# Kernel tuning notes

Measured on AMD Instinct MI355X. Metric: run time of the kernel, lower is better.

## Reference

```python
import jax, jax.numpy as jnp
import numpy as np

B, T, D, H, V = 256, 32, 500, 1024, 8000
NF = 512  # conv output channels per window size


def setup_inputs() -> dict:
    key = jax.random.key(0)
    ks = jax.random.split(key, 20)
    s = 0.02
    inp = {
        "text": jax.random.normal(ks[0], (B, T, D), jnp.float32),
        "text_bow": jax.random.uniform(ks[1], (B, V), jnp.float32),
        "text_lengths": jax.random.randint(ks[2], (B,), 1, T + 1).astype(jnp.int32),
        # GRU forward direction (PyTorch layout: [3H, D], [3H, H], gates r,z,n)
        "Wih_f": jax.random.normal(ks[3], (3 * H, D), jnp.float32) * s,
        "Whh_f": jax.random.normal(ks[4], (3 * H, H), jnp.float32) * s,
        "bih_f": jax.random.normal(ks[5], (3 * H,), jnp.float32) * s,
        "bhh_f": jax.random.normal(ks[6], (3 * H,), jnp.float32) * s,
        # GRU backward direction
        "Wih_b": jax.random.normal(ks[7], (3 * H, D), jnp.float32) * s,
        "Whh_b": jax.random.normal(ks[8], (3 * H, H), jnp.float32) * s,
        "bih_b": jax.random.normal(ks[9], (3 * H,), jnp.float32) * s,
        "bhh_b": jax.random.normal(ks[10], (3 * H,), jnp.float32) * s,
        # reduce linear: 2H -> H
        "W_red": jax.random.normal(ks[11], (H, 2 * H), jnp.float32) * s,
        "b_red": jax.random.normal(ks[12], (H,), jnp.float32) * s,
        # conv kernels, reshaped from Conv2d [512,1,ws,2H] to 1D conv [512, 2H, ws]
        "conv_w2": jax.random.normal(ks[13], (NF, 2 * H, 2), jnp.float32) * s,
        "conv_b2": jax.random.normal(ks[14], (NF,), jnp.float32) * s,
        "conv_w3": jax.random.normal(ks[15], (NF, 2 * H, 3), jnp.float32) * s,
        "conv_b3": jax.random.normal(ks[16], (NF,), jnp.float32) * s,
        "conv_w4": jax.random.normal(ks[17], (NF, 2 * H, 4), jnp.float32) * s,
        "conv_b4": jax.random.normal(ks[18], (NF,), jnp.float32) * s,
    }
    return inp


def _run_gru_dir(x, lengths, Wih, Whh, bih, bhh, reverse):
    """One GRU direction over padded [B,T,D] with packed-sequence semantics:
    outputs are zero at t >= length (as pad_packed_sequence produces)."""
    b, t, _ = x.shape
    h_dim = Whh.shape[1]
    xg = jnp.einsum('btd,gd->btg', x, Wih) + bih  # [B,T,3H] input projections
    valid = jnp.arange(t)[None, :] < lengths[:, None]  # [B,T]

    def step(h, inp):
        xg_t, v = inp  # [B,3H], [B]
        hg = h @ Whh.T + bhh
        xr, xz, xn = jnp.split(xg_t, 3, axis=-1)
        hr, hz, hn = jnp.split(hg, 3, axis=-1)
        r = jax.nn.sigmoid(xr + hr)
        z = jax.nn.sigmoid(xz + hz)
        n = jnp.tanh(xn + r * hn)
        h_new = (1.0 - z) * n + z * h
        h_new = jnp.where(v[:, None], h_new, h)
        out = jnp.where(v[:, None], h_new, 0.0)
        return h_new, out

    h0 = jnp.zeros((b, h_dim), x.dtype)
    xs = (jnp.swapaxes(xg, 0, 1), valid.T)  # time-major
    _, outs = jax.lax.scan(step, h0, xs, reverse=reverse)
    return jnp.swapaxes(outs, 0, 1)  # [B,T,H]


def _conv_branch(x_c, w, b, ws):
    # x_c: [B, 2H, T]; w: [512, 2H, ws]; 'same-padding-both-sides' (ws-1) like Conv2d padding=(ws-1,0)
    y = jax.lax.conv_general_dilated(
        x_c, w, window_strides=(1,), padding=[(ws - 1, ws - 1)],
        dimension_numbers=('NCH', 'OIH', 'NCH')) + b[None, :, None]
    y = jax.nn.leaky_relu(y, 0.01)
    return jnp.max(y, axis=-1)  # global max-pool over time -> [B,512]


def reference(text, text_bow, text_lengths, Wih_f, Whh_f, bih_f, bhh_f,
              Wih_b, Whh_b, bih_b, bhh_b, W_red, b_red,
              conv_w2, conv_b2, conv_w3, conv_b3, conv_w4, conv_b4):
    out_f = _run_gru_dir(text, text_lengths, Wih_f, Whh_f, bih_f, bhh_f, reverse=False)
    out_b = _run_gru_dir(text, text_lengths, Wih_b, Whh_b, bih_b, bhh_b, reverse=True)
    gru_init_out = jnp.concatenate([out_f, out_b], axis=-1)  # [B,T,2H]

    # masked mean pooling over valid timesteps (the per-sample Python loop)
    mask = (jnp.arange(gru_init_out.shape[1])[None, :] < text_lengths[:, None]).astype(gru_init_out.dtype)
    gru_mean = jnp.sum(gru_init_out * mask[:, :, None], axis=1) / text_lengths[:, None].astype(gru_init_out.dtype)
    gru_out = gru_mean @ W_red.T + b_red  # [B,H] (dropout is identity at eval)

    x_c = jnp.swapaxes(gru_init_out, 1, 2)  # [B,2H,T]
    con_out = jnp.concatenate([
        _conv_branch(x_c, conv_w2, conv_b2, 2),
        _conv_branch(x_c, conv_w3, conv_b3, 3),
        _conv_branch(x_c, conv_w4, conv_b4, 4),
    ], axis=1)  # [B,1536]

    return jnp.concatenate([gru_out, con_out, text_bow], axis=1)  # [B, H+1536+V]
```

## Files before the change

### kernel.cpp

```cpp
#include <hip/hip_runtime.h>
#include <hip/hip_bf16.h>
#include <math.h>

#define B_ 256
#define T_ 32
#define D_ 500
#define H_ 1024
#define V_ 8000
#define NF_ 512
#define G3H (3*H_)
#define G6H (6*H_)
#define H2 (2*H_)
#define OUTC (H_ + 3*NF_ + V_)
#define KPAD 512
#define NTAP 9
#define NCAT (NTAP*NF_)
#define MS 512
#define WFRAG_G (64*32*512)
#define WHH_N (3*64*32*64)

typedef float f32x4 __attribute__((ext_vector_type(4)));
typedef short bf16x8 __attribute__((ext_vector_type(8)));

static __device__ __forceinline__ short f2b(float f) {
    unsigned u = __float_as_uint(f);
    unsigned r = (u + 0x7fffu + ((u >> 16) & 1u)) >> 16;
    return (short)r;
}
static __device__ __forceinline__ float b2f(short s) {
    return __uint_as_float(((unsigned)(unsigned short)s) << 16);
}

__global__ __launch_bounds__(256) void gemm_bt(
    const short* __restrict__ A, int lda,
    const short* __restrict__ Bt, int ldb,
    const float* __restrict__ bias,
    void* __restrict__ Cv, int ldc,
    int K, int mode)
{
    __shared__ short As[128 * 32];
    __shared__ short Bs[128 * 32];
    const int tid  = threadIdx.x;
    const int w    = tid >> 6, lane = tid & 63;

    const int nbx = gridDim.x;
    const int nwg = nbx * gridDim.y;
    int flat = blockIdx.y * nbx + blockIdx.x;
    flat = (flat & 7) * (nwg >> 3) + (flat >> 3);
    const int m0 = (flat / nbx) * 128, n0 = (flat % nbx) * 128;

    const int wm   = (w >> 1) * 64, wn = (w & 1) * 64;

    f32x4 acc[4][4];
#pragma unroll
    for (int i = 0; i < 4; ++i)
#pragma unroll
        for (int j = 0; j < 4; ++j) acc[i][j] = (f32x4){0.f, 0.f, 0.f, 0.f};

    const int srow = w * 16 + (lane >> 2);
    const int scol = (lane & 3) * 8;
    const long aoff0 = (long)(m0 + srow) * lda + scol;
    const long aoff1 = (long)(m0 + srow + 64) * lda + scol;
    const long boff0 = (long)(n0 + srow) * ldb + scol;
    const long boff1 = (long)(n0 + srow + 64) * ldb + scol;
    short* lA0 = As + w * 512;        short* lA1 = As + 2048 + w * 512;
    short* lB0 = Bs + w * 512;        short* lB1 = Bs + 2048 + w * 512;

    const int fr = lane & 15, fk = (lane >> 4) * 8;

    for (int kt = 0; kt < K; kt += 32) {
        __builtin_amdgcn_global_load_lds((const __attribute__((address_space(1))) void*)(A + aoff0 + kt),
                                         (__attribute__((address_space(3))) void*)lA0, 16, 0, 0);
        __builtin_amdgcn_global_load_lds((const __attribute__((address_space(1))) void*)(A + aoff1 + kt),
                                         (__attribute__((address_space(3))) void*)lA1, 16, 0, 0);
        __builtin_amdgcn_global_load_lds((const __attribute__((address_space(1))) void*)(Bt + boff0 + kt),
                                         (__attribute__((address_space(3))) void*)lB0, 16, 0, 0);
        __builtin_amdgcn_global_load_lds((const __attribute__((address_space(1))) void*)(Bt + boff1 + kt),
                                         (__attribute__((address_space(3))) void*)lB1, 16, 0, 0);
        __syncthreads();
        bf16x8 af[4], bfv[4];
#pragma unroll
        for (int i = 0; i < 4; ++i) af[i]  = *(const bf16x8*)(As + (wm + i * 16 + fr) * 32 + fk);
#pragma unroll
        for (int j = 0; j < 4; ++j) bfv[j] = *(const bf16x8*)(Bs + (wn + j * 16 + fr) * 32 + fk);
#pragma unroll
        for (int i = 0; i < 4; ++i)
#pragma unroll
            for (int j = 0; j < 4; ++j)
                acc[i][j] = __builtin_amdgcn_mfma_f32_16x16x32_bf16(af[i], bfv[j], acc[i][j], 0, 0, 0);
        __syncthreads();
    }

    const int er = (lane >> 4) * 4;
    const int ec = lane & 15;
#pragma unroll
    for (int i = 0; i < 4; ++i) {
#pragma unroll
        for (int j = 0; j < 4; ++j) {
#pragma unroll
            for (int q = 0; q < 4; ++q) {
                const int m = m0 + wm + i * 16 + er + q;
                const int n = n0 + wn + j * 16 + ec;
                float v = acc[i][j][q];
                if (mode == 0) {
                    ((float*)Cv)[(long)m * ldc + n] = v + bias[n];
                } else if (mode == 2) {
                    ((short*)Cv)[(long)m * ldc + n] = f2b(v + bias[n]);
                } else {
                    ((_Float16*)Cv)[(long)m * ldc + n] = (_Float16)v;
                }
            }
        }
    }
}

__global__ void repack_whh2(const float* __restrict__ srcf,
                            const float* __restrict__ srcb,
                            short* __restrict__ dst)
{
    const int idx = blockIdx.x * 256 + threadIdx.x;
    const int h = idx >= WHH_N;
    const int local = idx - h * WHH_N;
    const float* src = h ? srcb : srcf;
    const int l = local & 63;
    const int kt = (local >> 6) & 31;
    const int j16 = (local >> 11) & 63;
    const int g = local >> 17;
    const long srow = ((long)(g << 10) + (j16 << 4) + (l & 15)) * H_ + kt * 32 + ((l >> 4) << 3);
    short o[8];
#pragma unroll
    for (int e = 0; e < 8; ++e) o[e] = f2b(src[srow + e]);
    *(bf16x8*)&dst[(long)idx * 8] = *(bf16x8*)o;
}

__global__ __launch_bounds__(512) void gru_step_frag(
    const short* __restrict__ hbf_prev, short* __restrict__ hbf_next,
    const float* __restrict__ h32_prev, float* __restrict__ h32_next,
    const short* __restrict__ wfragf, const short* __restrict__ wfragb,
    const float* __restrict__ bhhf, const float* __restrict__ bhhb,
    const short* __restrict__ xgcat,
    short* __restrict__ gout, const int* __restrict__ lengths, int s)
{
    __shared__ f32x4 lacc[4][6][64];
    const int tid = threadIdx.x;
    const int w8 = tid >> 6;
    const int w = w8 & 3;
    const int khalf = w8 >> 2;
    const int lane = tid & 63;
    const int bid = blockIdx.x;
    const int jt = bid & 31;
    const int mtd = bid >> 5;
    const int dir = mtd >> 2, mt = mtd & 3;
    const int m0 = dir * 256 + mt * 64;
    const int j0 = jt * 32;
    const int wm = (w >> 1) * 32, wj = (w & 1) * 16;
    const int tt = dir ? (T_ - 1 - s) : s;

    const short* wfrag = dir ? wfragb : wfragf;
    const float* bhh = dir ? bhhb : bhhf;

    const int fr15 = lane & 15, fk8 = (lane >> 4) * 8;
    const long arow0 = (long)(m0 + wm + fr15) * H_ + fk8 + khalf * 512;
    const long arow1 = arow0 + (long)16 * H_;
    const int j16 = (j0 + wj) >> 4;
    const short* bbase = wfrag + ((long)j16 * 32 + khalf * 16) * 512 + lane * 8;

    f32x4 acc[3][2];
#pragma unroll
    for (int g = 0; g < 3; ++g)
#pragma unroll
        for (int i = 0; i < 2; ++i) acc[g][i] = (f32x4){0.f, 0.f, 0.f, 0.f};

#pragma unroll 4
    for (int kt = 0; kt < 16; ++kt) {
        const bf16x8 af0 = *(const bf16x8*)(hbf_prev + arow0 + kt * 32);
        const bf16x8 af1 = *(const bf16x8*)(hbf_prev + arow1 + kt * 32);
        const bf16x8 b0 = *(const bf16x8*)(bbase + (long)kt * 512);
        const bf16x8 b1 = *(const bf16x8*)(bbase + (long)kt * 512 + WFRAG_G);
        const bf16x8 b2 = *(const bf16x8*)(bbase + (long)kt * 512 + 2 * WFRAG_G);
        acc[0][0] = __builtin_amdgcn_mfma_f32_16x16x32_bf16(af0, b0, acc[0][0], 0, 0, 0);
        acc[0][1] = __builtin_amdgcn_mfma_f32_16x16x32_bf16(af1, b0, acc[0][1], 0, 0, 0);
        acc[1][0] = __builtin_amdgcn_mfma_f32_16x16x32_bf16(af0, b1, acc[1][0], 0, 0, 0);
        acc[1][1] = __builtin_amdgcn_mfma_f32_16x16x32_bf16(af1, b1, acc[1][1], 0, 0, 0);
        acc[2][0] = __builtin_amdgcn_mfma_f32_16x16x32_bf16(af0, b2, acc[2][0], 0, 0, 0);
        acc[2][1] = __builtin_amdgcn_mfma_f32_16x16x32_bf16(af1, b2, acc[2][1], 0, 0, 0);
    }

    if (khalf == 1) {
#pragma unroll
        for (int g = 0; g < 3; ++g)
#pragma unroll
            for (int i = 0; i < 2; ++i)
                lacc[w][g * 2 + i][lane] = acc[g][i];
    }
    __syncthreads();
    if (khalf == 1) return;

#pragma unroll
    for (int g = 0; g < 3; ++g)
#pragma unroll
        for (int i = 0; i < 2; ++i)
            acc[g][i] += lacc[w][g * 2 + i][lane];

    const int er = (lane >> 4) * 4, ec = lane & 15;
    const int jj = j0 + wj + ec;
    const float bhr = bhh[jj], bhz = bhh[H_ + jj], bhn = bhh[2 * H_ + jj];

#pragma unroll
    for (int i = 0; i < 2; ++i) {
#pragma unroll
        for (int q = 0; q < 4; ++q) {
            const int m = m0 + wm + i * 16 + er + q;
            const int b = m & 255;
            const short* xrow = xgcat + ((long)b * T_ + tt) * G6H + (long)dir * G3H;
            const float xr = b2f(xrow[jj]);
            const float xz = b2f(xrow[H_ + jj]);
            const float xn = b2f(xrow[2 * H_ + jj]);
            const float rr = 1.f / (1.f + expf(-(xr + acc[0][i][q] + bhr)));
            const float zz = 1.f / (1.f + expf(-(xz + acc[1][i][q] + bhz)));
            const float nn = tanhf(xn + rr * (acc[2][i][q] + bhn));
            const long hidx = (long)m * H_ + jj;
            const float hp = h32_prev[hidx];
            const float hnew = (1.f - zz) * nn + zz * hp;
            const bool valid = tt < lengths[b];
            const float ho = valid ? hnew : hp;
            h32_next[hidx] = ho;
            hbf_next[hidx] = f2b(ho);
            gout[((long)b * T_ + tt) * H2 + (long)dir * H_ + jj] = valid ? f2b(hnew) : (short)0;
        }
    }
}

__global__ void f2b_pad(const float* __restrict__ src, short* __restrict__ dst,
                        int Ksrc, int Kdst)
{
    const int idx = blockIdx.x * 256 + threadIdx.x;
    const int r = idx / Kdst, c = idx % Kdst;
    dst[idx] = (c < Ksrc) ? f2b(src[(long)r * Ksrc + c]) : (short)0;
}

__global__ void wih_pad2(const float* __restrict__ a, const float* __restrict__ b,
                         short* __restrict__ dst)
{
    const int idx = blockIdx.x * 256 + threadIdx.x;
    const int h = idx >= G3H * KPAD;
    const int rem = idx - h * G3H * KPAD;
    const int r = rem / KPAD, c = rem % KPAD;
    const float* s = h ? b : a;
    dst[idx] = (c < D_) ? f2b(s[(long)r * D_ + c]) : (short)0;
}

__global__ void cat_bias(const float* __restrict__ a, const float* __restrict__ b,
                         float* __restrict__ dst)
{
    const int idx = blockIdx.x * 256 + threadIdx.x;
    dst[idx] = (idx < G3H) ? a[idx] : b[idx - G3H];
}

__global__ void repack_tap_all(const float* __restrict__ cw2,
                               const float* __restrict__ cw3,
                               const float* __restrict__ cw4,
                               short* __restrict__ dst)
{
    const int idx = blockIdx.x * 256 + threadIdx.x;
    const int tap = idx / (NF_ * H2);
    const int rem = idx % (NF_ * H2);
    const int f = rem >> 11, c = rem & 2047;
    const float* src; int ws, k;
    if (tap < 2)      { src = cw2; ws = 2; k = tap; }
    else if (tap < 5) { src = cw3; ws = 3; k = tap - 2; }
    else              { src = cw4; ws = 4; k = tap - 5; }
    dst[idx] = f2b(src[((long)(f << 11) + c) * ws + k]);
}

__global__ void mean_pool2(const short* __restrict__ gin,
                           const int* __restrict__ lengths,
                           short* __restrict__ mean_bf)
{
    const int idx = blockIdx.x * 256 + threadIdx.x;
    const int b = idx >> 11, c = idx & 2047;
    float s = 0.f;
#pragma unroll
    for (int t = 0; t < T_; ++t) s += b2f(gin[((long)(b * T_ + t)) * H2 + c]);
    mean_bf[idx] = f2b(s / (float)lengths[b]);
}

__global__ void conv_max(const _Float16* __restrict__ P,
                         const float* __restrict__ cb2, const float* __restrict__ cb3,
                         const float* __restrict__ cb4, float* __restrict__ out)
{
    const int idx = blockIdx.x * 256 + threadIdx.x;
    const int b = idx / 1536, u0 = idx % 1536;
    int Tout, ws, base, f; float bias;
    if (u0 < 512)       { ws = 2; Tout = 33; base = 0;    f = u0;        bias = cb2[f]; }
    else if (u0 < 1024) { ws = 3; Tout = 34; base = 1024; f = u0 - 512;  bias = cb3[f]; }
    else                { ws = 4; Tout = 35; base = 2560; f = u0 - 1024; bias = cb4[f]; }
    const _Float16* Pb = P + (long)b * T_ * NCAT + base + f;
    float m = -INFINITY;
    for (int u = 0; u < Tout; ++u) {
        float s = bias;
        for (int k = 0; k < ws; ++k) {
            const int t = u - (ws - 1) + k;
            if (t >= 0 && t < T_) s += (float)Pb[(long)t * NCAT + k * NF_];
        }
        s = s > 0.f ? s : 0.01f * s;
        m = fmaxf(m, s);
    }
    out[(long)b * OUTC + H_ + u0] = m;
}

__global__ void bow_copy(const float* __restrict__ bow, float* __restrict__ out)
{
    const int idx = blockIdx.x * 256 + threadIdx.x;
    const int b = idx / 2000, q = idx % 2000;
    const float4* src = (const float4*)(bow + (long)b * V_);
    float4* dst = (float4*)(out + (long)b * OUTC + H_ + 3 * NF_);
    dst[q] = src[q];
}

extern "C" void kernel_launch(void* const* d_in, const int* in_sizes, int n_in,
                              void* d_out, int out_size, void* d_ws, size_t ws_size,
                              hipStream_t stream)
{
    const float* text    = (const float*)d_in[0];
    const float* bow     = (const float*)d_in[1];
    const int*   lengths = (const int*)  d_in[2];
    const float* Wih_f   = (const float*)d_in[3];
    const float* Whh_f   = (const float*)d_in[4];
    const float* bih_f   = (const float*)d_in[5];
    const float* bhh_f   = (const float*)d_in[6];
    const float* Wih_b   = (const float*)d_in[7];
    const float* Whh_b   = (const float*)d_in[8];
    const float* bih_b   = (const float*)d_in[9];
    const float* bhh_b   = (const float*)d_in[10];
    const float* W_red   = (const float*)d_in[11];
    const float* b_red   = (const float*)d_in[12];
    const float* cw2     = (const float*)d_in[13];
    const float* cb2     = (const float*)d_in[14];
    const float* cw3     = (const float*)d_in[15];
    const float* cb3     = (const float*)d_in[16];
    const float* cw4     = (const float*)d_in[17];
    const float* cb4     = (const float*)d_in[18];
    float* out = (float*)d_out;

    char* ws = (char*)d_ws;
    size_t off = 0;
    short* xgcat = (short*)(ws + off); off += (size_t)B_ * T_ * G6H * 2;
    _Float16* P    = (_Float16*)(char*)xgcat;
    short* wtap_bf = (short*)((char*)xgcat + (size_t)B_ * T_ * NCAT * 2);
    short* gin_bf = (short*)(ws + off); off += (size_t)B_ * T_ * H2 * 2;
    short* text_bf = gin_bf;
    short* wih_bf  = (short*)((char*)gin_bf + (size_t)B_ * T_ * KPAD * 2);
    short* wfrag   = (short*)(ws + off); off += (size_t)2 * 3 * WFRAG_G * 2;
    short* wfragf  = wfrag;
    short* wfragb  = wfrag + (size_t)3 * WFRAG_G;
    short* wred_bf = (short*)(ws + off); off += (size_t)H_ * H2 * 2;
    float* h32     = (float*)(ws + off); off += (size_t)2 * MS * H_ * 4;
    short* h_bf    = (short*)(ws + off); off += (size_t)2 * MS * H_ * 2;
    short* gmean_bf= (short*)(ws + off); off += (size_t)B_ * H2 * 2;
    float* bih_cat = (float*)(ws + off); off += (size_t)G6H * 4;

    const dim3 blk(256);

    f2b_pad<<<dim3((B_ * T_ * KPAD) / 256), blk, 0, stream>>>(text, text_bf, D_, KPAD);
    wih_pad2<<<dim3((2 * G3H * KPAD) / 256), blk, 0, stream>>>(Wih_f, Wih_b, wih_bf);
    f2b_pad<<<dim3((H_ * H2) / 256), blk, 0, stream>>>(W_red, wred_bf, H2, H2);
    cat_bias<<<dim3(G6H / 256), blk, 0, stream>>>(bih_f, bih_b, bih_cat);
    repack_whh2<<<dim3((2 * WHH_N) / 256), blk, 0, stream>>>(Whh_f, Whh_b, wfrag);

    gemm_bt<<<dim3(G6H / 128, (B_ * T_) / 128), blk, 0, stream>>>(
        text_bf, KPAD, wih_bf, KPAD, bih_cat, xgcat, G6H, KPAD, 2);

    hipMemsetAsync(h32, 0, (size_t)MS * H_ * 4, stream);
    hipMemsetAsync(h_bf, 0, (size_t)MS * H_ * 2, stream);
    for (int s = 0; s < T_; ++s) {
        const int cur = s & 1, nxt = (s + 1) & 1;
        gru_step_frag<<<dim3(256), dim3(512), 0, stream>>>(
            h_bf + (size_t)cur * MS * H_, h_bf + (size_t)nxt * MS * H_,
            h32 + (size_t)cur * MS * H_, h32 + (size_t)nxt * MS * H_,
            wfragf, wfragb, bhh_f, bhh_b, xgcat,
            gin_bf, lengths, s);
    }

    mean_pool2<<<dim3((B_ * H2) / 256), blk, 0, stream>>>(gin_bf, lengths, gmean_bf);
    gemm_bt<<<dim3(H_ / 128, B_ / 128), blk, 0, stream>>>(
        gmean_bf, H2, wred_bf, H2, b_red, out, OUTC, H2, 0);

    repack_tap_all<<<dim3((NTAP * NF_ * H2) / 256), blk, 0, stream>>>(cw2, cw3, cw4, wtap_bf);
    gemm_bt<<<dim3(NCAT / 128, (B_ * T_) / 128), blk, 0, stream>>>(
        gin_bf, H2, wtap_bf, H2, nullptr, P, NCAT, H2, 3);

    conv_max<<<dim3((B_ * 1536) / 256), blk, 0, stream>>>(P, cb2, cb3, cb4, out);
    bow_copy<<<dim3((B_ * 2000) / 256), blk, 0, stream>>>(bow, out);
}
```

Before: 1.033 ms.

## Add triple-buffered direct-to-LDS GEMM for input projection and conv taps

Adds a templated GEMM that loads A and B tiles straight from global memory into LDS with global_load_lds, using three buffers with a two-tile prefetch and swizzled addresses. It replaces the old GEMM for the GRU input projection and the conv-tap GEMM. The aim is to overlap global loads with MFMA compute and skip the register staging copy. This uses more LDS, which may lower occupancy. The epilogue is specialised at compile time per mode.

```diff
diff --git a/kernel.cpp b/kernel.cpp
--- a/kernel.cpp
+++ b/kernel.cpp
@@ -29,6 +29,109 @@
 }
 static __device__ __forceinline__ float b2f(short s) {
     return __uint_as_float(((unsigned)(unsigned short)s) << 16);
+}
+
+template<int MODE>
+__global__ __launch_bounds__(256) void gemm_bt2(
+    const short* __restrict__ A, int lda,
+    const short* __restrict__ Bt, int ldb,
+    const float* __restrict__ bias,
+    void* __restrict__ Cv, int ldc, int K)
+{
+    __shared__ short As[3][128 * 32];
+    __shared__ short Bs[3][128 * 32];
+    const int tid = threadIdx.x;
+    const int w = tid >> 6, lane = tid & 63;
+
+    const int nbx = gridDim.x;
+    const int nwg = nbx * gridDim.y;
+    int flat = blockIdx.y * nbx + blockIdx.x;
+    flat = (flat & 7) * (nwg >> 3) + (flat >> 3);
+    const int m0 = (flat / nbx) * 128, n0 = (flat % nbx) * 128;
+
+    const int wm = (w >> 1) * 64, wn = (w & 1) * 64;
+
+    const int sa = lane & 1, sb = (lane >> 1) & 1, sc = (lane >> 2) & 1;
+    const int sd = (lane >> 3) & 1, se = (lane >> 4) & 1, sg = (lane >> 5) & 1;
+    const int srow = w * 16 + (sc ^ sg) + 2 * sd + 4 * se + 8 * sg;
+    const int scol = 8 * ((sa ^ sd) + 2 * (sb ^ se));
+    const long aoff0 = (long)(m0 + srow) * lda + scol;
+    const long aoff1 = (long)(m0 + srow + 64) * lda + scol;
+    const long boff0 = (long)(n0 + srow) * ldb + scol;
+    const long boff1 = (long)(n0 + srow + 64) * ldb + scol;
+
+#define STG(t_) do { \
+    const int bu_ = (t_) % 3; \
+    const long ka_ = (long)(t_) * 32; \
+    __builtin_amdgcn_global_load_lds((const __attribute__((address_space(1))) void*)(A + aoff0 + ka_), \
+        (__attribute__((address_space(3))) void*)(&As[bu_][w * 512]), 16, 0, 0); \
+    __builtin_amdgcn_global_load_lds((const __attribute__((address_space(1))) void*)(A + aoff1 + ka_), \
+        (__attribute__((address_space(3))) void*)(&As[bu_][2048 + w * 512]), 16, 0, 0); \
+    __builtin_amdgcn_global_load_lds((const __attribute__((address_space(1))) void*)(Bt + boff0 + ka_), \
+        (__attribute__((address_space(3))) void*)(&Bs[bu_][w * 512]), 16, 0, 0); \
+    __builtin_amdgcn_global_load_lds((const __attribute__((address_space(1))) void*)(Bt + boff1 + ka_), \
+        (__attribute__((address_space(3))) void*)(&Bs[bu_][2048 + w * 512]), 16, 0, 0); \
+} while (0)
+
+    f32x4 acc[4][4];
+#pragma unroll
+    for (int i = 0; i < 4; ++i)
+#pragma unroll
+        for (int j = 0; j < 4; ++j) acc[i][j] = (f32x4){0.f, 0.f, 0.f, 0.f};
+
+    const int fr = lane & 15;
+    const int fkb = (lane >> 4) * 16;
+    const int fxor = ((fr >> 1) & 7) << 4;
+    const int T = K >> 5;
+
+    STG(0); STG(1);
+    asm volatile("s_waitcnt vmcnt(4)" ::: "memory");
+    __builtin_amdgcn_s_barrier();
+
+    for (int t = 0; t < T; ++t) {
+        const int bu = t % 3;
+        const char* Ab = (const char*)&As[bu][0];
+        const char* Bb = (const char*)&Bs[bu][0];
+
+        bf16x8 af[4], bfv[4];
+#pragma unroll
+        for (int i = 0; i < 4; ++i)
+            af[i] = *(const bf16x8*)(Ab + ((((wm + i * 16 + fr) << 6) + fkb) ^ fxor));
+#pragma unroll
+        for (int j = 0; j < 4; ++j)
+            bfv[j] = *(const bf16x8*)(Bb + ((((wn + j * 16 + fr) << 6) + fkb) ^ fxor));
+
+        if (t + 2 < T) STG(t + 2);
+
+#pragma unroll
+        for (int i = 0; i < 4; ++i)
+#pragma unroll
+            for (int j = 0; j < 4; ++j)
+                acc[i][j] = __builtin_amdgcn_mfma_f32_16x16x32_bf16(af[i], bfv[j], acc[i][j], 0, 0, 0);
+
+        if (t + 2 < T)      asm volatile("s_waitcnt vmcnt(4)" ::: "memory");
+        else if (t + 1 < T) asm volatile("s_waitcnt vmcnt(0)" ::: "memory");
+        __builtin_amdgcn_s_barrier();
+    }
+#undef STG
+
+    const int er = (lane >> 4) * 4, ec = lane & 15;
+#pragma unroll
+    for (int i = 0; i < 4; ++i) {
+#pragma unroll
+        for (int j = 0; j < 4; ++j) {
+#pragma unroll
+            for (int q = 0; q < 4; ++q) {
+                const int m = m0 + wm + i * 16 + er + q;
+                const int n = n0 + wn + j * 16 + ec;
+                const float v = acc[i][j][q];
+                if (MODE == 2)
+                    ((short*)Cv)[(long)m * ldc + n] = f2b(v + bias[n]);
+                else
+                    ((_Float16*)Cv)[(long)m * ldc + n] = (_Float16)v;
+            }
+        }
+    }
 }
 
 __global__ __launch_bounds__(256) void gemm_bt(
@@ -368,8 +471,8 @@
     cat_bias<<<dim3(G6H / 256), blk, 0, stream>>>(bih_f, bih_b, bih_cat);
     repack_whh2<<<dim3((2 * WHH_N) / 256), blk, 0, stream>>>(Whh_f, Whh_b, wfrag);
 
-    gemm_bt<<<dim3(G6H / 128, (B_ * T_) / 128), blk, 0, stream>>>(
-        text_bf, KPAD, wih_bf, KPAD, bih_cat, xgcat, G6H, KPAD, 2);
+    gemm_bt2<2><<<dim3(G6H / 128, (B_ * T_) / 128), blk, 0, stream>>>(
+        text_bf, KPAD, wih_bf, KPAD, bih_cat, xgcat, G6H, KPAD);
 
     hipMemsetAsync(h32, 0, (size_t)MS * H_ * 4, stream);
     hipMemsetAsync(h_bf, 0, (size_t)MS * H_ * 2, stream);
@@ -387,8 +490,8 @@
         gmean_bf, H2, wred_bf, H2, b_red, out, OUTC, H2, 0);
 
     repack_tap_all<<<dim3((NTAP * NF_ * H2) / 256), blk, 0, stream>>>(cw2, cw3, cw4, wtap_bf);
-    gemm_bt<<<dim3(NCAT / 128, (B_ * T_) / 128), blk, 0, stream>>>(
-        gin_bf, H2, wtap_bf, H2, nullptr, P, NCAT, H2, 3);
+    gemm_bt2<3><<<dim3(NCAT / 128, (B_ * T_) / 128), blk, 0, stream>>>(
+        gin_bf, H2, wtap_bf, H2, nullptr, P, NCAT, H2);
 
     conv_max<<<dim3((B_ * 1536) / 256), blk, 0, stream>>>(P, cb2, cb3, cb4, out);
     bow_copy<<<dim3((B_ * 2000) / 256), blk, 0, stream>>>(bow, out);
```

Result: faster. 958.4 us (-7.2%).
